# Optimization experiments

Measured on AMD Instinct MI355X. Metric: run time of the kernel, lower is better.

The kernel has to match this reference:

```python
import jax, jax.numpy as jnp
import numpy as np

N = 50000      # nodes
E = 800000     # edges (avg degree 16)
F_IN = 128     # num_features
H1 = 256       # hidden_dims[0]
H2 = 128       # hidden_dims[1]
D_EMB = 64     # embedding_dim
C_CLS = 2      # num_classes
EPS = 1e-5     # BatchNorm eps


def setup_inputs() -> dict:
    key = jax.random.key(0)
    ks = jax.random.split(key, 24)
    f32 = jnp.float32
    def w(k, shape, scale=0.05):
        return jax.random.normal(k, shape, f32) * scale
    inp = {
        "x": jax.random.normal(ks[0], (N, F_IN), f32),
        "edge_index": jax.random.randint(ks[1], (2, E), 0, N, jnp.int32),
        # input_proj
        "Wp": w(ks[2], (F_IN, H1)), "bp": jnp.zeros((H1,), f32),
        # conv1 (SAGEConv): lin_l (neighbors, with bias), lin_r (root, no bias)
        "W1l": w(ks[3], (F_IN, H1)), "b1l": jnp.zeros((H1,), f32), "W1r": w(ks[4], (F_IN, H1)),
        # bn1 (eval mode, running stats)
        "bn1_g": jnp.ones((H1,), f32), "bn1_b": jnp.zeros((H1,), f32),
        "bn1_m": w(ks[5], (H1,), 0.01), "bn1_v": jnp.ones((H1,), f32) + 0.1 * jax.random.uniform(ks[6], (H1,), f32),
        # skip_proj
        "Wsk": w(ks[7], (H1, H2)), "bsk": jnp.zeros((H2,), f32),
        # conv2
        "W2l": w(ks[8], (H1, H2)), "b2l": jnp.zeros((H2,), f32), "W2r": w(ks[9], (H1, H2)),
        # bn2
        "bn2_g": jnp.ones((H2,), f32), "bn2_b": jnp.zeros((H2,), f32),
        "bn2_m": w(ks[10], (H2,), 0.01), "bn2_v": jnp.ones((H2,), f32) + 0.1 * jax.random.uniform(ks[11], (H2,), f32),
        # conv3
        "W3l": w(ks[12], (H2, D_EMB)), "b3l": jnp.zeros((D_EMB,), f32), "W3r": w(ks[13], (H2, D_EMB)),
        # classifier
        "Wc": w(ks[14], (D_EMB, C_CLS)), "bc": jnp.zeros((C_CLS,), f32),
    }
    return inp


def _sage(h, src, dst, Wl, bl, Wr):
    # mean aggregation of source features into destination nodes
    s = jax.ops.segment_sum(h[src], dst, num_segments=N)        # [N, d]
    cnt = jax.ops.segment_sum(jnp.ones((src.shape[0], 1), h.dtype), dst, num_segments=N)
    mean = s / jnp.maximum(cnt, 1.0)
    return mean @ Wl + bl + h @ Wr


def _bn(h, g, b, m, v):
    return (h - m) * jax.lax.rsqrt(v + EPS) * g + b


def reference(x, edge_index, Wp, bp, W1l, b1l, W1r, bn1_g, bn1_b, bn1_m, bn1_v,
              Wsk, bsk, W2l, b2l, W2r, bn2_g, bn2_b, bn2_m, bn2_v,
              W3l, b3l, W3r, Wc, bc):
    src, dst = edge_index[0], edge_index[1]
    identity = x @ Wp + bp                                # input_proj
    h = _sage(x, src, dst, W1l, b1l, W1r)                 # conv1
    h = jax.nn.relu(_bn(h, bn1_g, bn1_b, bn1_m, bn1_v) + identity)
    # dropout is identity in eval mode
    identity = h @ Wsk + bsk                              # skip_proj
    h = _sage(h, src, dst, W2l, b2l, W2r)                 # conv2
    h = jax.nn.relu(_bn(h, bn2_g, bn2_b, bn2_m, bn2_v) + identity)
    emb = _sage(h, src, dst, W3l, b3l, W3r)               # conv3
    logits = emb @ Wc + bc
    return (logits, emb)
```

## Files before the change

kernel.cpp:

```cpp
#include <hip/hip_runtime.h>
#include <hip/hip_fp16.h>

#define NN 50000
#define NE 800000
#define SLN 6250
#define CAP 64
#define BCAP 106496
constexpr float EPSV = 1e-5f;

typedef __attribute__((ext_vector_type(8))) short short8;
typedef __attribute__((ext_vector_type(4))) float f32x4;

__device__ __forceinline__ float bf2f(unsigned short u) {
    return __uint_as_float(((unsigned int)u) << 16);
}
__device__ __forceinline__ unsigned short f2bf(float f) {
    unsigned int x = __float_as_uint(f);
    return (unsigned short)((x + 0x7FFFu + ((x >> 16) & 1u)) >> 16);
}
__device__ __forceinline__ unsigned char f2e5(float f) {
    unsigned short h = __half_as_ushort(__float2half(f));
    unsigned short r = h + 0x7F + ((h >> 8) & 1);
    return (unsigned char)(r >> 8);
}
__device__ __forceinline__ void acc16(float* a, uint4 u) {
#pragma unroll
    for (int q = 0; q < 4; q++) {
        unsigned int x = (q == 0) ? u.x : (q == 1) ? u.y : (q == 2) ? u.z : u.w;
        unsigned int h01 = ((x << 8) & 0xFF00u) | ((x << 16) & 0xFF000000u);
        unsigned int h23 = ((x >> 8) & 0xFF00u) | (x & 0xFF000000u);
        __half2 p01 = *(__half2*)&h01, p23 = *(__half2*)&h23;
        float2 f01 = __half22float2(p01), f23 = __half22float2(p23);
        a[q * 4 + 0] += f01.x; a[q * 4 + 1] += f01.y;
        a[q * 4 + 2] += f23.x; a[q * 4 + 3] += f23.y;
    }
}

__global__ __launch_bounds__(256) void k_bin(const int* __restrict__ src,
                                             const int* __restrict__ dst,
                                             int* __restrict__ binCnt,
                                             int2* __restrict__ binBuf) {
    __shared__ int hcnt[8];
    __shared__ int hbase[8];
    int tid = threadIdx.x;
    if (tid < 8) hcnt[tid] = 0;
    __syncthreads();
    int q = blockIdx.x * 256 + tid;
    bool val = q < NE / 4;
    int4 d = make_int4(0, 0, 0, 0), s = make_int4(0, 0, 0, 0);
    int b0 = 0, b1 = 0, b2 = 0, b3 = 0, r0 = 0, r1 = 0, r2 = 0, r3 = 0;
    if (val) {
        d = ((const int4*)dst)[q];
        s = ((const int4*)src)[q];
        b0 = d.x / SLN; r0 = atomicAdd(&hcnt[b0], 1);
        b1 = d.y / SLN; r1 = atomicAdd(&hcnt[b1], 1);
        b2 = d.z / SLN; r2 = atomicAdd(&hcnt[b2], 1);
        b3 = d.w / SLN; r3 = atomicAdd(&hcnt[b3], 1);
    }
    __syncthreads();
    if (tid < 8) hbase[tid] = atomicAdd(&binCnt[tid], hcnt[tid]);
    __syncthreads();
    if (val) {
        binBuf[(size_t)b0 * BCAP + hbase[b0] + r0] = make_int2(d.x, s.x);
        binBuf[(size_t)b1 * BCAP + hbase[b1] + r1] = make_int2(d.y, s.y);
        binBuf[(size_t)b2 * BCAP + hbase[b2] + r2] = make_int2(d.z, s.z);
        binBuf[(size_t)b3 * BCAP + hbase[b3] + r3] = make_int2(d.w, s.w);
    }
}

__global__ __launch_bounds__(256) void k_scatter2(const int2* __restrict__ binBuf,
                                                  const int* __restrict__ binCnt,
                                                  int* __restrict__ cnt,
                                                  int* __restrict__ csr) {
    int bin = blockIdx.x & 7;
    int lb = blockIdx.x >> 3;
    int n = binCnt[bin];
    const int2* buf = binBuf + (size_t)bin * BCAP;
    for (int i = lb * 256 + threadIdx.x; i < n; i += 128 * 256) {
        int2 p = buf[i];
        int slot = atomicAdd(&cnt[p.x], 1);
        csr[p.x * CAP + slot] = p.y;
    }
}

__device__ void prep1_body(int t, const float* Wp, const float* bp, const float* W1l,
                           const float* b1l, const float* W1r, const float* g, const float* b,
                           const float* m, const float* v, unsigned short* Wf, float* c) {
    int lane = t & 63, f = (t >> 6) & 3, kt = (t >> 8) & 7;
    int nb = t >> 11;
    int col = nb * 64 + f * 16 + (lane & 15);
    int k0 = kt * 32 + (lane >> 4) * 8;
    float A = g[col] * rsqrtf(v[col] + EPSV);
    unsigned short* o = Wf + (size_t)t * 8;
    for (int j = 0; j < 8; j++) {
        int k = k0 + j;
        float w;
        if (k < 128) w = W1l[k * 256 + col] * A;
        else         w = W1r[(k - 128) * 256 + col] * A + Wp[(k - 128) * 256 + col];
        o[j] = f2bf(w);
    }
    if (t < 256) {
        float At = g[t] * rsqrtf(v[t] + EPSV);
        c[t] = b1l[t] * At + (b[t] - m[t] * At) + bp[t];
    }
}

__device__ void prep2_body(int t, const float* Wsk, const float* bsk, const float* W2l,
                           const float* b2l, const float* W2r, const float* g, const float* b,
                           const float* m, const float* v, unsigned short* Wf, float* c) {
    int lane = t & 63, f = (t >> 6) & 3, kt = (t >> 8) & 7, nb = t >> 11;
    int col = nb * 64 + f * 16 + (lane & 15);
    int k0 = kt * 32 + (lane >> 4) * 8;
    unsigned short* o = Wf + (size_t)t * 8;
    if (col < 128) {
        float A = g[col] * rsqrtf(v[col] + EPSV);
        for (int j = 0; j < 8; j++) o[j] = f2bf(W2l[(k0 + j) * 128 + col] * A);
    } else {
        int cc = col - 128;
        float A = g[cc] * rsqrtf(v[cc] + EPSV);
        for (int j = 0; j < 8; j++)
            o[j] = f2bf(W2r[(k0 + j) * 128 + cc] * A + Wsk[(k0 + j) * 128 + cc]);
    }
    if (t < 128) {
        float At = g[t] * rsqrtf(v[t] + EPSV);
        c[t] = b2l[t] * At + (b[t] - m[t] * At) + bsk[t];
    }
}

__device__ void prep3_body(int t, const float* W3l, const float* b3l, const float* W3r,
                           unsigned short* Wf, float* c) {
    int lane = t & 63, f = (t >> 6) & 3, kt = (t >> 8) & 3, nb = t >> 10;
    int col = nb * 64 + f * 16 + (lane & 15);
    int k0 = kt * 32 + (lane >> 4) * 8;
    unsigned short* o = Wf + (size_t)t * 8;
    if (col < 64) {
        for (int j = 0; j < 8; j++) o[j] = f2bf(W3l[(k0 + j) * 64 + col]);
    } else {
        int cc = col - 64;
        for (int j = 0; j < 8; j++) o[j] = f2bf(W3r[(k0 + j) * 64 + cc]);
    }
    if (t < 64) c[t] = b3l[t];
}

__global__ void k_prep_fused(const float* x, unsigned short* xcat, unsigned char* xf8,
                             int* cnt, int* binCnt,
                             const float* Wp, const float* bp,
                             const float* W1l, const float* b1l, const float* W1r,
                             const float* g1, const float* b1, const float* m1, const float* v1,
                             const float* Wsk, const float* bsk,
                             const float* W2l, const float* b2l, const float* W2r,
                             const float* g2, const float* b2, const float* m2, const float* v2,
                             const float* W3l, const float* b3l, const float* W3r,
                             unsigned short* Wf1, unsigned short* Wf2, unsigned short* Wf3,
                             float* c1, float* c2, float* c3) {
    int bb = blockIdx.x;
    if (bb < 6250) {
        int i = bb * 256 + threadIdx.x;
        if (i < NN / 4) ((int4*)cnt)[i] = make_int4(0, 0, 0, 0);
        if (i < 2) ((int4*)binCnt)[i] = make_int4(0, 0, 0, 0);
        if (i >= NN * 128 / 4) return;
        int r = i >> 5, c4 = (i & 31) * 4;
        float4 v = ((const float4*)x)[i];
        ushort4 u = make_ushort4(f2bf(v.x), f2bf(v.y), f2bf(v.z), f2bf(v.w));
        *(ushort4*)&xcat[(size_t)r * 256 + 128 + c4] = u;
        uchar4 u8 = make_uchar4(f2e5(v.x), f2e5(v.y), f2e5(v.z), f2e5(v.w));
        *(uchar4*)&xf8[(size_t)r * 128 + c4] = u8;
    } else if (bb < 6282) {
        prep1_body((bb - 6250) * 256 + threadIdx.x, Wp, bp, W1l, b1l, W1r, g1, b1, m1, v1, Wf1, c1);
    } else if (bb < 6314) {
        prep2_body((bb - 6282) * 256 + threadIdx.x, Wsk, bsk, W2l, b2l, W2r, g2, b2, m2, v2, Wf2, c2);
    } else {
        prep3_body((bb - 6314) * 256 + threadIdx.x, W3l, b3l, W3r, Wf3, c3);
    }
}

template <int K, int TOTN, int MODE>
__global__ __launch_bounds__(256) void k_gemm(const unsigned short* __restrict__ A,
                                              const unsigned short* __restrict__ Wf,
                                              const float* __restrict__ bias,
                                              unsigned short* __restrict__ Out,
                                              unsigned char* __restrict__ Pf8) {
    constexpr int KT = K / 32;
    constexpr int NB = TOTN / 64;
    __shared__ unsigned short Bs[K * 64];
    int tid = threadIdx.x;
    int lane = tid & 63, w = tid >> 6;
    int bm = blockIdx.x;

    int r0 = bm * 128 + w * 32;
    int ra0 = r0 + (lane & 15);
    int ra1 = ra0 + 16;
    if (ra0 >= NN) ra0 = NN - 1;
    if (ra1 >= NN) ra1 = NN - 1;
    const unsigned short* ap0 = A + (size_t)ra0 * K + ((lane >> 4) * 8);
    const unsigned short* ap1 = A + (size_t)ra1 * K + ((lane >> 4) * 8);
    short8 afr0[KT], afr1[KT];
#pragma unroll
    for (int kt = 0; kt < KT; kt++) {
        afr0[kt] = *(const short8*)(ap0 + kt * 32);
        afr1[kt] = *(const short8*)(ap1 + kt * 32);
    }

    int rb = r0 + (lane >> 4) * 4;

    for (int nb = 0; nb < NB; nb++) {
        __syncthreads();
        {
            const float4* srcp = (const float4*)(Wf + (size_t)nb * K * 64);
            float4* dsts = (float4*)Bs;
            for (int i = tid; i < K * 8; i += 256) dsts[i] = srcp[i];
        }
        __syncthreads();

        f32x4 acc[2][4];
#pragma unroll
        for (int i = 0; i < 2; i++)
#pragma unroll
            for (int f = 0; f < 4; f++) acc[i][f] = (f32x4){0.f, 0.f, 0.f, 0.f};
#pragma unroll
        for (int kt = 0; kt < KT; kt++) {
#pragma unroll
            for (int f = 0; f < 4; f++) {
                short8 bfr = *(const short8*)&Bs[((kt * 4 + f) * 64 + lane) * 8];
                acc[0][f] = __builtin_amdgcn_mfma_f32_16x16x32_bf16(afr0[kt], bfr, acc[0][f], 0, 0, 0);
                acc[1][f] = __builtin_amdgcn_mfma_f32_16x16x32_bf16(afr1[kt], bfr, acc[1][f], 0, 0, 0);
            }
        }

        int cc = nb * 64 + (lane & 15);
#pragma unroll
        for (int af = 0; af < 2; af++) {
#pragma unroll
            for (int f = 0; f < 4; f++) {
                float bv = (MODE == 1) ? bias[cc + f * 16] : 0.f;
#pragma unroll
                for (int r = 0; r < 4; r++) {
                    int gr = rb + af * 16 + r;
                    if (gr < NN) {
                        float val = acc[af][f][r];
                        if (MODE == 1) val = fmaxf(val + bv, 0.f);
                        int col = cc + f * 16;
                        if (MODE == 2) {
                            if (col < 128) Pf8[(size_t)gr * 128 + col] = f2e5(val);
                            else           Out[(size_t)gr * 128 + (col - 128)] = f2bf(val);
                        } else {
                            Out[(size_t)gr * TOTN + col] = f2bf(val);
                        }
                    }
                }
            }
        }
    }
}


__global__ __launch_bounds__(256) void k_aggx(const int* __restrict__ cnt,
                                              const int* __restrict__ csr,
                                              const unsigned char* __restrict__ xf8,
                                              unsigned short* __restrict__ xcat) {
    int lane = threadIdx.x & 63, wv = threadIdx.x >> 6;
    int node = blockIdx.x * 4 + wv;
    int deg = cnt[node];
    const int* cp = csr + node * CAP;
    int g = lane >> 3, l8 = lane & 7;
    float a[16];
#pragma unroll
    for (int j = 0; j < 16; j++) a[j] = 0.f;
    const unsigned char* base = xf8 + l8 * 16;
    int e = 0;
    for (; e + 16 <= deg; e += 16) {
        int s0 = cp[e + g], s1 = cp[e + 8 + g];
        uint4 u0 = *(const uint4*)(base + (size_t)s0 * 128);
        uint4 u1 = *(const uint4*)(base + (size_t)s1 * 128);
        acc16(a, u0); acc16(a, u1);
    }
    if (e + g < deg) {
        uint4 u = *(const uint4*)(base + (size_t)cp[e + g] * 128);
        acc16(a, u);
    }
    if (e + 8 + g < deg) {
        uint4 u = *(const uint4*)(base + (size_t)cp[e + 8 + g] * 128);
        acc16(a, u);
    }
#pragma unroll
    for (int j = 0; j < 16; j++) {
        a[j] += __shfl_xor(a[j], 8);
        a[j] += __shfl_xor(a[j], 16);
        a[j] += __shfl_xor(a[j], 32);
    }
    if (lane < 8) {
        float inv = 1.f / (float)max(deg, 1);
        unsigned short o[16];
#pragma unroll
        for (int j = 0; j < 16; j++) o[j] = f2bf(a[j] * inv);
        *(short8*)&xcat[(size_t)node * 256 + lane * 16] = *(short8*)&o[0];
        *(short8*)&xcat[(size_t)node * 256 + lane * 16 + 8] = *(short8*)&o[8];
    }
}

__global__ __launch_bounds__(256) void k_agg2(const unsigned char* __restrict__ pf8,
                                              const unsigned short* __restrict__ r2,
                                              const int* __restrict__ cnt,
                                              const int* __restrict__ csr,
                                              const float* __restrict__ c,
                                              unsigned short* __restrict__ h2) {
    int lane = threadIdx.x & 63, wv = threadIdx.x >> 6;
    int node = blockIdx.x * 4 + wv;
    int deg = cnt[node];
    const int* cp = csr + node * CAP;
    int g = lane >> 3, l8 = lane & 7;
    float a[16];
#pragma unroll
    for (int j = 0; j < 16; j++) a[j] = 0.f;
    const unsigned char* base = pf8 + l8 * 16;
    int e = 0;
    for (; e + 16 <= deg; e += 16) {
        int s0 = cp[e + g], s1 = cp[e + 8 + g];
        uint4 u0 = *(const uint4*)(base + (size_t)s0 * 128);
        uint4 u1 = *(const uint4*)(base + (size_t)s1 * 128);
        acc16(a, u0); acc16(a, u1);
    }
    if (e + g < deg) {
        uint4 u = *(const uint4*)(base + (size_t)cp[e + g] * 128);
        acc16(a, u);
    }
    if (e + 8 + g < deg) {
        uint4 u = *(const uint4*)(base + (size_t)cp[e + 8 + g] * 128);
        acc16(a, u);
    }
#pragma unroll
    for (int j = 0; j < 16; j++) {
        a[j] += __shfl_xor(a[j], 8);
        a[j] += __shfl_xor(a[j], 16);
        a[j] += __shfl_xor(a[j], 32);
    }
    if (lane < 8) {
        float inv = 1.f / (float)max(deg, 1);
        short8 rA = *(const short8*)&r2[(size_t)node * 128 + lane * 16];
        short8 rB = *(const short8*)&r2[(size_t)node * 128 + lane * 16 + 8];
        const float* cpb = c + lane * 16;
        unsigned short o[16];
#pragma unroll
        for (int j = 0; j < 8; j++)
            o[j] = f2bf(fmaxf(a[j] * inv + bf2f(rA[j]) + cpb[j], 0.f));
#pragma unroll
        for (int j = 0; j < 8; j++)
            o[8 + j] = f2bf(fmaxf(a[8 + j] * inv + bf2f(rB[j]) + cpb[8 + j], 0.f));
        *(short8*)&h2[(size_t)node * 128 + lane * 16] = *(short8*)&o[0];
        *(short8*)&h2[(size_t)node * 128 + lane * 16 + 8] = *(short8*)&o[8];
    }
}

__global__ __launch_bounds__(256) void k_agg_final(const unsigned short* __restrict__ G,
                                                   const int* __restrict__ cnt,
                                                   const int* __restrict__ csr,
                                                   const float* __restrict__ c,
                                                   const float* __restrict__ Wc,
                                                   const float* __restrict__ bc,
                                                   float* __restrict__ outbuf) {
    int lane = threadIdx.x & 63, wv = threadIdx.x >> 6;
    int node = blockIdx.x * 4 + wv;
    int deg = cnt[node];
    const int* cp = csr + node * CAP;
    int g = lane >> 3, l8 = lane & 7;
    float a[8];
#pragma unroll
    for (int j = 0; j < 8; j++) a[j] = 0.f;
    const unsigned short* base = G + l8 * 8;
    int e = 0;
    for (; e + 32 <= deg; e += 32) {
        int s0 = cp[e + g], s1 = cp[e + 8 + g], s2 = cp[e + 16 + g], s3 = cp[e + 24 + g];
        short8 u0 = *(const short8*)(base + (size_t)s0 * 128);
        short8 u1 = *(const short8*)(base + (size_t)s1 * 128);
        short8 u2 = *(const short8*)(base + (size_t)s2 * 128);
        short8 u3 = *(const short8*)(base + (size_t)s3 * 128);
#pragma unroll
        for (int j = 0; j < 8; j++)
            a[j] += (bf2f(u0[j]) + bf2f(u1[j])) + (bf2f(u2[j]) + bf2f(u3[j]));
    }
    for (; e + 8 <= deg; e += 8) {
        short8 u = *(const short8*)(base + (size_t)cp[e + g] * 128);
#pragma unroll
        for (int j = 0; j < 8; j++) a[j] += bf2f(u[j]);
    }
    if (e + g < deg) {
        short8 u = *(const short8*)(base + (size_t)cp[e + g] * 128);
#pragma unroll
        for (int j = 0; j < 8; j++) a[j] += bf2f(u[j]);
    }
#pragma unroll
    for (int j = 0; j < 8; j++) {
        a[j] += __shfl_xor(a[j], 8);
        a[j] += __shfl_xor(a[j], 16);
        a[j] += __shfl_xor(a[j], 32);
    }
    float l0 = 0.f, l1 = 0.f;
    if (lane < 8) {
        float inv = 1.f / (float)max(deg, 1);
        short8 r = *(const short8*)&G[(size_t)node * 128 + 64 + l8 * 8];
        const float* cpb = c + l8 * 8;
        float v[8];
#pragma unroll
        for (int j = 0; j < 8; j++) v[j] = a[j] * inv + bf2f(r[j]) + cpb[j];
        float* emb = outbuf + 2 * (size_t)NN;
        *(float4*)&emb[(size_t)node * 64 + l8 * 8] = make_float4(v[0], v[1], v[2], v[3]);
        *(float4*)&emb[(size_t)node * 64 + l8 * 8 + 4] = make_float4(v[4], v[5], v[6], v[7]);
        int c0 = l8 * 8;
#pragma unroll
        for (int j = 0; j < 8; j++) {
            l0 += v[j] * Wc[2 * (c0 + j)];
            l1 += v[j] * Wc[2 * (c0 + j) + 1];
        }
    }
    l0 += __shfl_xor(l0, 1); l1 += __shfl_xor(l1, 1);
    l0 += __shfl_xor(l0, 2); l1 += __shfl_xor(l1, 2);
    l0 += __shfl_xor(l0, 4); l1 += __shfl_xor(l1, 4);
    if (lane == 0) {
        outbuf[(size_t)node * 2 + 0] = l0 + bc[0];
        outbuf[(size_t)node * 2 + 1] = l1 + bc[1];
    }
}

extern "C" void kernel_launch(void* const* d_in, const int* in_sizes, int n_in,
                              void* d_out, int out_size, void* d_ws, size_t ws_size,
                              hipStream_t stream) {
    const float* x    = (const float*)d_in[0];
    const int*   ei   = (const int*)d_in[1];
    const float* Wp   = (const float*)d_in[2];
    const float* bp   = (const float*)d_in[3];
    const float* W1l  = (const float*)d_in[4];
    const float* b1l  = (const float*)d_in[5];
    const float* W1r  = (const float*)d_in[6];
    const float* bn1g = (const float*)d_in[7];
    const float* bn1b = (const float*)d_in[8];
    const float* bn1m = (const float*)d_in[9];
    const float* bn1v = (const float*)d_in[10];
    const float* Wsk  = (const float*)d_in[11];
    const float* bsk  = (const float*)d_in[12];
    const float* W2l  = (const float*)d_in[13];
    const float* b2l  = (const float*)d_in[14];
    const float* W2r  = (const float*)d_in[15];
    const float* bn2g = (const float*)d_in[16];
    const float* bn2b = (const float*)d_in[17];
    const float* bn2m = (const float*)d_in[18];
    const float* bn2v = (const float*)d_in[19];
    const float* W3l  = (const float*)d_in[20];
    const float* b3l  = (const float*)d_in[21];
    const float* W3r  = (const float*)d_in[22];
    const float* Wc   = (const float*)d_in[23];
    const float* bc   = (const float*)d_in[24];

    const int* src = ei;
    const int* dst = ei + NE;

    char* ws = (char*)d_ws;
    size_t o = 0;
    auto alloc = [&](size_t b) -> char* {
        char* p = ws + o;
        o = (o + b + 255) & ~(size_t)255;
        return p;
    };
    int* cnt    = (int*)alloc((size_t)NN * 4);
    int* binCnt = (int*)alloc(64);
    int* csr    = (int*)alloc((size_t)NN * CAP * 4);
    unsigned char*  xf8  = (unsigned char*)alloc((size_t)NN * 128);
    unsigned short* xcat = (unsigned short*)alloc((size_t)NN * 256 * 2);
    unsigned short* h1   = (unsigned short*)alloc((size_t)NN * 256 * 2);
    unsigned char*  pf8  = (unsigned char*)alloc((size_t)NN * 128);
    unsigned short* r2   = (unsigned short*)alloc((size_t)NN * 128 * 2);
    unsigned short* h2   = (unsigned short*)alloc((size_t)NN * 128 * 2);
    unsigned short* G3   = (unsigned short*)alloc((size_t)NN * 128 * 2);
    unsigned short* Wf1  = (unsigned short*)alloc((size_t)256 * 256 * 2);
    unsigned short* Wf2  = (unsigned short*)alloc((size_t)256 * 256 * 2);
    unsigned short* Wf3  = (unsigned short*)alloc((size_t)128 * 128 * 2);
    float* c1 = (float*)alloc(256 * 4);
    float* c2 = (float*)alloc(128 * 4);
    float* c3 = (float*)alloc(64 * 4);
    int2* binBuf = (int2*)G3;

    float* outbuf = (float*)d_out;

    k_prep_fused<<<6322, 256, 0, stream>>>(x, xcat, xf8, cnt, binCnt,
                                           Wp, bp, W1l, b1l, W1r, bn1g, bn1b, bn1m, bn1v,
                                           Wsk, bsk, W2l, b2l, W2r, bn2g, bn2b, bn2m, bn2v,
                                           W3l, b3l, W3r, Wf1, Wf2, Wf3, c1, c2, c3);

    k_bin<<<782, 256, 0, stream>>>(src, dst, binCnt, binBuf);
    k_scatter2<<<1024, 256, 0, stream>>>(binBuf, binCnt, cnt, csr);

    k_aggx<<<12500, 256, 0, stream>>>(cnt, csr, xf8, xcat);
    k_gemm<256, 256, 1><<<391, 256, 0, stream>>>(xcat, Wf1, c1, h1, nullptr);

    k_gemm<256, 256, 2><<<391, 256, 0, stream>>>(h1, Wf2, nullptr, r2, pf8);
    k_agg2<<<12500, 256, 0, stream>>>(pf8, r2, cnt, csr, c2, h2);

    k_gemm<128, 128, 0><<<391, 256, 0, stream>>>(h2, Wf3, nullptr, G3, nullptr);
    k_agg_final<<<12500, 256, 0, stream>>>(G3, cnt, csr, c3, Wc, bc, outbuf);
}
```

Before: 210.8 us.

## Fuse conv1 and conv2 GEMMs into one kernel keeping h1 in LDS

Adds a kernel that runs the layer-1 GEMM (bias+ReLU) for a 64-row tile, stores the bf16 h1 tile in padded shared memory, and feeds it straight into the layer-2 GEMM that writes pf8/r2. This removes the global round trip of the N×256 bf16 h1 buffer and one kernel launch. In exchange the tiles are smaller (64 rows per block, 782 blocks), both weight matrices are re-streamed through LDS per block, LDS use per block rises, and the generic GEMM loses its MODE-specific epilogues.

New measurement: 200.2 us (median of 2 runs). 1.05x faster.

```diff
diff --git a/kernel.cpp b/kernel.cpp
--- a/kernel.cpp
+++ b/kernel.cpp
@@ -174,6 +174,106 @@
     }
 }
 
+__global__ __launch_bounds__(256) void k_gemm12(const unsigned short* __restrict__ xcat,
+                                                const unsigned short* __restrict__ Wf1,
+                                                const float* __restrict__ c1,
+                                                const unsigned short* __restrict__ Wf2,
+                                                unsigned short* __restrict__ r2,
+                                                unsigned char* __restrict__ pf8) {
+    constexpr int KT = 8;
+    constexpr int HS = 272;
+    __shared__ unsigned short Bs[256 * 64];
+    __shared__ unsigned short hs[64 * HS];
+    int tid = threadIdx.x;
+    int lane = tid & 63, w = tid >> 6;
+    int bm = blockIdx.x;
+    int rbase = bm * 64 + w * 16;
+
+    int ra = rbase + (lane & 15);
+    if (ra >= NN) ra = NN - 1;
+    const unsigned short* ap = xcat + (size_t)ra * 256 + ((lane >> 4) * 8);
+    short8 afr[KT];
+#pragma unroll
+    for (int kt = 0; kt < KT; kt++) afr[kt] = *(const short8*)(ap + kt * 32);
+
+    int hrow0 = w * 16 + (lane >> 4) * 4;
+
+    for (int nb = 0; nb < 4; nb++) {
+        __syncthreads();
+        {
+            const float4* srcp = (const float4*)(Wf1 + (size_t)nb * 256 * 64);
+            float4* dsts = (float4*)Bs;
+            for (int i = tid; i < 256 * 8; i += 256) dsts[i] = srcp[i];
+        }
+        __syncthreads();
+        f32x4 acc[4];
+#pragma unroll
+        for (int f = 0; f < 4; f++) acc[f] = (f32x4){0.f, 0.f, 0.f, 0.f};
+#pragma unroll
+        for (int kt = 0; kt < KT; kt++) {
+#pragma unroll
+            for (int f = 0; f < 4; f++) {
+                short8 bfr = *(const short8*)&Bs[((kt * 4 + f) * 64 + lane) * 8];
+                acc[f] = __builtin_amdgcn_mfma_f32_16x16x32_bf16(afr[kt], bfr, acc[f], 0, 0, 0);
+            }
+        }
+        int cc = nb * 64 + (lane & 15);
+#pragma unroll
+        for (int f = 0; f < 4; f++) {
+            int col = cc + f * 16;
+            float bv = c1[col];
+#pragma unroll
+            for (int r = 0; r < 4; r++) {
+                float val = fmaxf(acc[f][r] + bv, 0.f);
+                hs[(hrow0 + r) * HS + col] = f2bf(val);
+            }
+        }
+    }
+
+    short8 a2[KT];
+    {
+        const unsigned short* hp = &hs[(w * 16 + (lane & 15)) * HS + ((lane >> 4) * 8)];
+#pragma unroll
+        for (int kt = 0; kt < KT; kt++) a2[kt] = *(const short8*)(hp + kt * 32);
+    }
+
+    int gr0 = rbase + (lane >> 4) * 4;
+    for (int nb = 0; nb < 4; nb++) {
+        __syncthreads();
+        {
+            const float4* srcp = (const float4*)(Wf2 + (size_t)nb * 256 * 64);
+            float4* dsts = (float4*)Bs;
+            for (int i = tid; i < 256 * 8; i += 256) dsts[i] = srcp[i];
+        }
+        __syncthreads();
+        f32x4 acc[4];
+#pragma unroll
+        for (int f = 0; f < 4; f++) acc[f] = (f32x4){0.f, 0.f, 0.f, 0.f};
+#pragma unroll
+        for (int kt = 0; kt < KT; kt++) {
+#pragma unroll
+            for (int f = 0; f < 4; f++) {
+                short8 bfr = *(const short8*)&Bs[((kt * 4 + f) * 64 + lane) * 8];
+                acc[f] = __builtin_amdgcn_mfma_f32_16x16x32_bf16(a2[kt], bfr, acc[f], 0, 0, 0);
+            }
+        }
+        int cc = nb * 64 + (lane & 15);
+#pragma unroll
+        for (int f = 0; f < 4; f++) {
+            int col = cc + f * 16;
+#pragma unroll
+            for (int r = 0; r < 4; r++) {
+                int gr = gr0 + r;
+                if (gr < NN) {
+                    float val = acc[f][r];
+                    if (col < 128) pf8[(size_t)gr * 128 + col] = f2e5(val);
+                    else           r2[(size_t)gr * 128 + (col - 128)] = f2bf(val);
+                }
+            }
+        }
+    }
+}
+
 template <int K, int TOTN, int MODE>
 __global__ __launch_bounds__(256) void k_gemm(const unsigned short* __restrict__ A,
                                               const unsigned short* __restrict__ Wf,
@@ -232,20 +332,12 @@
         for (int af = 0; af < 2; af++) {
 #pragma unroll
             for (int f = 0; f < 4; f++) {
-                float bv = (MODE == 1) ? bias[cc + f * 16] : 0.f;
 #pragma unroll
                 for (int r = 0; r < 4; r++) {
                     int gr = rb + af * 16 + r;
                     if (gr < NN) {
                         float val = acc[af][f][r];
-                        if (MODE == 1) val = fmaxf(val + bv, 0.f);
-                        int col = cc + f * 16;
-                        if (MODE == 2) {
-                            if (col < 128) Pf8[(size_t)gr * 128 + col] = f2e5(val);
-                            else           Out[(size_t)gr * 128 + (col - 128)] = f2bf(val);
-                        } else {
-                            Out[(size_t)gr * TOTN + col] = f2bf(val);
-                        }
+                        Out[(size_t)gr * TOTN + cc + f * 16] = f2bf(val);
                     }
                 }
             }
@@ -465,7 +557,6 @@
     int* csr    = (int*)alloc((size_t)NN * CAP * 4);
     unsigned char*  xf8  = (unsigned char*)alloc((size_t)NN * 128);
     unsigned short* xcat = (unsigned short*)alloc((size_t)NN * 256 * 2);
-    unsigned short* h1   = (unsigned short*)alloc((size_t)NN * 256 * 2);
     unsigned char*  pf8  = (unsigned char*)alloc((size_t)NN * 128);
     unsigned short* r2   = (unsigned short*)alloc((size_t)NN * 128 * 2);
     unsigned short* h2   = (unsigned short*)alloc((size_t)NN * 128 * 2);
@@ -489,9 +580,8 @@
     k_scatter2<<<1024, 256, 0, stream>>>(binBuf, binCnt, cnt, csr);
 
     k_aggx<<<12500, 256, 0, stream>>>(cnt, csr, xf8, xcat);
-    k_gemm<256, 256, 1><<<391, 256, 0, stream>>>(xcat, Wf1, c1, h1, nullptr);
-
-    k_gemm<256, 256, 2><<<391, 256, 0, stream>>>(h1, Wf2, nullptr, r2, pf8);
+
+    k_gemm12<<<782, 256, 0, stream>>>(xcat, Wf1, c1, Wf2, r2, pf8);
     k_agg2<<<12500, 256, 0, stream>>>(pf8, r2, cnt, csr, c2, h2);
 
     k_gemm<128, 128, 0><<<391, 256, 0, stream>>>(h2, Wf3, nullptr, G3, nullptr);
```

## Fuse edge binning into prep kernel and split GEMM column blocks across grid

Applied to the files above, without the earlier changes.

Folds the edge-binning kernel into the fused prep kernel as extra blocks, zeroing binCnt with a memset beforehand. The two 256-wide GEMMs now put each 64-column block in its own grid.y slice instead of looping over it, which gives four times as many blocks at the cost of reloading A fragments per slice. The third GEMM becomes a dedicated kernel with 64-row tiles to double its block count. The aim is more parallelism and one fewer launch, in exchange for redundant A reads and an extra memset.

Result: slower. 222.6 us (+5.6%).

```diff
diff --git a/kernel.cpp b/kernel.cpp
--- a/kernel.cpp
+++ b/kernel.cpp
@@ -33,38 +33,6 @@
         float2 f01 = __half22float2(p01), f23 = __half22float2(p23);
         a[q * 4 + 0] += f01.x; a[q * 4 + 1] += f01.y;
         a[q * 4 + 2] += f23.x; a[q * 4 + 3] += f23.y;
-    }
-}
-
-__global__ __launch_bounds__(256) void k_bin(const int* __restrict__ src,
-                                             const int* __restrict__ dst,
-                                             int* __restrict__ binCnt,
-                                             int2* __restrict__ binBuf) {
-    __shared__ int hcnt[8];
-    __shared__ int hbase[8];
-    int tid = threadIdx.x;
-    if (tid < 8) hcnt[tid] = 0;
-    __syncthreads();
-    int q = blockIdx.x * 256 + tid;
-    bool val = q < NE / 4;
-    int4 d = make_int4(0, 0, 0, 0), s = make_int4(0, 0, 0, 0);
-    int b0 = 0, b1 = 0, b2 = 0, b3 = 0, r0 = 0, r1 = 0, r2 = 0, r3 = 0;
-    if (val) {
-        d = ((const int4*)dst)[q];
-        s = ((const int4*)src)[q];
-        b0 = d.x / SLN; r0 = atomicAdd(&hcnt[b0], 1);
-        b1 = d.y / SLN; r1 = atomicAdd(&hcnt[b1], 1);
-        b2 = d.z / SLN; r2 = atomicAdd(&hcnt[b2], 1);
-        b3 = d.w / SLN; r3 = atomicAdd(&hcnt[b3], 1);
-    }
-    __syncthreads();
-    if (tid < 8) hbase[tid] = atomicAdd(&binCnt[tid], hcnt[tid]);
-    __syncthreads();
-    if (val) {
-        binBuf[(size_t)b0 * BCAP + hbase[b0] + r0] = make_int2(d.x, s.x);
-        binBuf[(size_t)b1 * BCAP + hbase[b1] + r1] = make_int2(d.y, s.y);
-        binBuf[(size_t)b2 * BCAP + hbase[b2] + r2] = make_int2(d.z, s.z);
-        binBuf[(size_t)b3 * BCAP + hbase[b3] + r3] = make_int2(d.w, s.w);
     }
 }
 
@@ -144,6 +112,7 @@
 
 __global__ void k_prep_fused(const float* x, unsigned short* xcat, unsigned char* xf8,
                              int* cnt, int* binCnt,
+                             const int* src, const int* dst, int2* binBuf,
                              const float* Wp, const float* bp,
                              const float* W1l, const float* b1l, const float* W1r,
                              const float* g1, const float* b1, const float* m1, const float* v1,
@@ -153,11 +122,13 @@
                              const float* W3l, const float* b3l, const float* W3r,
                              unsigned short* Wf1, unsigned short* Wf2, unsigned short* Wf3,
                              float* c1, float* c2, float* c3) {
+    __shared__ int hcnt[8];
+    __shared__ int hbase[8];
     int bb = blockIdx.x;
+    int tid = threadIdx.x;
     if (bb < 6250) {
-        int i = bb * 256 + threadIdx.x;
+        int i = bb * 256 + tid;
         if (i < NN / 4) ((int4*)cnt)[i] = make_int4(0, 0, 0, 0);
-        if (i < 2) ((int4*)binCnt)[i] = make_int4(0, 0, 0, 0);
         if (i >= NN * 128 / 4) return;
         int r = i >> 5, c4 = (i & 31) * 4;
         float4 v = ((const float4*)x)[i];
@@ -166,11 +137,35 @@
         uchar4 u8 = make_uchar4(f2e5(v.x), f2e5(v.y), f2e5(v.z), f2e5(v.w));
         *(uchar4*)&xf8[(size_t)r * 128 + c4] = u8;
     } else if (bb < 6282) {
-        prep1_body((bb - 6250) * 256 + threadIdx.x, Wp, bp, W1l, b1l, W1r, g1, b1, m1, v1, Wf1, c1);
+        prep1_body((bb - 6250) * 256 + tid, Wp, bp, W1l, b1l, W1r, g1, b1, m1, v1, Wf1, c1);
     } else if (bb < 6314) {
-        prep2_body((bb - 6282) * 256 + threadIdx.x, Wsk, bsk, W2l, b2l, W2r, g2, b2, m2, v2, Wf2, c2);
+        prep2_body((bb - 6282) * 256 + tid, Wsk, bsk, W2l, b2l, W2r, g2, b2, m2, v2, Wf2, c2);
+    } else if (bb < 6322) {
+        prep3_body((bb - 6314) * 256 + tid, W3l, b3l, W3r, Wf3, c3);
     } else {
-        prep3_body((bb - 6314) * 256 + threadIdx.x, W3l, b3l, W3r, Wf3, c3);
+        if (tid < 8) hcnt[tid] = 0;
+        __syncthreads();
+        int q = (bb - 6322) * 256 + tid;
+        bool val = q < NE / 4;
+        int4 d = make_int4(0, 0, 0, 0), s = make_int4(0, 0, 0, 0);
+        int b0 = 0, b1i = 0, b2i = 0, b3i = 0, r0 = 0, r1 = 0, r2 = 0, r3 = 0;
+        if (val) {
+            d = ((const int4*)dst)[q];
+            s = ((const int4*)src)[q];
+            b0 = d.x / SLN; r0 = atomicAdd(&hcnt[b0], 1);
+            b1i = d.y / SLN; r1 = atomicAdd(&hcnt[b1i], 1);
+            b2i = d.z / SLN; r2 = atomicAdd(&hcnt[b2i], 1);
+            b3i = d.w / SLN; r3 = atomicAdd(&hcnt[b3i], 1);
+        }
+        __syncthreads();
+        if (tid < 8) hbase[tid] = atomicAdd(&binCnt[tid], hcnt[tid]);
+        __syncthreads();
+        if (val) {
+            binBuf[(size_t)b0 * BCAP + hbase[b0] + r0] = make_int2(d.x, s.x);
+            binBuf[(size_t)b1i * BCAP + hbase[b1i] + r1] = make_int2(d.y, s.y);
+            binBuf[(size_t)b2i * BCAP + hbase[b2i] + r2] = make_int2(d.z, s.z);
+            binBuf[(size_t)b3i * BCAP + hbase[b3i] + r3] = make_int2(d.w, s.w);
+        }
     }
 }
 
@@ -181,11 +176,10 @@
                                               unsigned short* __restrict__ Out,
                                               unsigned char* __restrict__ Pf8) {
     constexpr int KT = K / 32;
-    constexpr int NB = TOTN / 64;
     __shared__ unsigned short Bs[K * 64];
     int tid = threadIdx.x;
     int lane = tid & 63, w = tid >> 6;
-    int bm = blockIdx.x;
+    int bm = blockIdx.x, nb = blockIdx.y;
 
     int r0 = bm * 128 + w * 32;
     int ra0 = r0 + (lane & 15);
@@ -201,53 +195,98 @@
         afr1[kt] = *(const short8*)(ap1 + kt * 32);
     }
 
+    {
+        const float4* srcp = (const float4*)(Wf + (size_t)nb * K * 64);
+        float4* dsts = (float4*)Bs;
+        for (int i = tid; i < K * 8; i += 256) dsts[i] = srcp[i];
+    }
+    __syncthreads();
+
+    f32x4 acc[2][4];
+#pragma unroll
+    for (int i = 0; i < 2; i++)
+#pragma unroll
+        for (int f = 0; f < 4; f++) acc[i][f] = (f32x4){0.f, 0.f, 0.f, 0.f};
+#pragma unroll
+    for (int kt = 0; kt < KT; kt++) {
+#pragma unroll
+        for (int f = 0; f < 4; f++) {
+            short8 bfr = *(const short8*)&Bs[((kt * 4 + f) * 64 + lane) * 8];
+            acc[0][f] = __builtin_amdgcn_mfma_f32_16x16x32_bf16(afr0[kt], bfr, acc[0][f], 0, 0, 0);
+            acc[1][f] = __builtin_amdgcn_mfma_f32_16x16x32_bf16(afr1[kt], bfr, acc[1][f], 0, 0, 0);
+        }
+    }
+
+    int cc = nb * 64 + (lane & 15);
     int rb = r0 + (lane >> 4) * 4;
-
-    for (int nb = 0; nb < NB; nb++) {
+#pragma unroll
+    for (int af = 0; af < 2; af++) {
+#pragma unroll
+        for (int f = 0; f < 4; f++) {
+            int col = cc + f * 16;
+            float bv = (MODE == 1) ? bias[col] : 0.f;
+#pragma unroll
+            for (int r = 0; r < 4; r++) {
+                int gr = rb + af * 16 + r;
+                if (gr < NN) {
+                    float val = acc[af][f][r];
+                    if (MODE == 1) {
+                        val = fmaxf(val + bv, 0.f);
+                        Out[(size_t)gr * TOTN + col] = f2bf(val);
+                    } else {
+                        if (col < 128) Pf8[(size_t)gr * 128 + col] = f2e5(val);
+                        else           Out[(size_t)gr * 128 + (col - 128)] = f2bf(val);
+                    }
+                }
+            }
+        }
+    }
+}
+
+__global__ __launch_bounds__(256) void k_gemm3(const unsigned short* __restrict__ h2,
+                                               const unsigned short* __restrict__ Wf3,
+                                               unsigned short* __restrict__ G3) {
+    constexpr int KT = 4;
+    __shared__ unsigned short Bs[128 * 64];
+    int tid = threadIdx.x;
+    int lane = tid & 63, w = tid >> 6;
+    int bm = blockIdx.x;
+
+    int ra = bm * 64 + w * 16 + (lane & 15);
+    if (ra >= NN) ra = NN - 1;
+    const unsigned short* ap = h2 + (size_t)ra * 128 + ((lane >> 4) * 8);
+    short8 afr[KT];
+#pragma unroll
+    for (int kt = 0; kt < KT; kt++) afr[kt] = *(const short8*)(ap + kt * 32);
+
+    int gr0 = bm * 64 + w * 16 + (lane >> 4) * 4;
+
+    for (int nb = 0; nb < 2; nb++) {
         __syncthreads();
         {
-            const float4* srcp = (const float4*)(Wf + (size_t)nb * K * 64);
+            const float4* srcp = (const float4*)(Wf3 + (size_t)nb * 128 * 64);
             float4* dsts = (float4*)Bs;
-            for (int i = tid; i < K * 8; i += 256) dsts[i] = srcp[i];
+            for (int i = tid; i < 128 * 8; i += 256) dsts[i] = srcp[i];
         }
         __syncthreads();
-
-        f32x4 acc[2][4];
-#pragma unroll
-        for (int i = 0; i < 2; i++)
-#pragma unroll
-            for (int f = 0; f < 4; f++) acc[i][f] = (f32x4){0.f, 0.f, 0.f, 0.f};
+        f32x4 acc[4];
+#pragma unroll
+        for (int f = 0; f < 4; f++) acc[f] = (f32x4){0.f, 0.f, 0.f, 0.f};
 #pragma unroll
         for (int kt = 0; kt < KT; kt++) {
 #pragma unroll
             for (int f = 0; f < 4; f++) {
                 short8 bfr = *(const short8*)&Bs[((kt * 4 + f) * 64 + lane) * 8];
-                acc[0][f] = __builtin_amdgcn_mfma_f32_16x16x32_bf16(afr0[kt], bfr, acc[0][f], 0, 0, 0);
-                acc[1][f] = __builtin_amdgcn_mfma_f32_16x16x32_bf16(afr1[kt], bfr, acc[1][f], 0, 0, 0);
+                acc[f] = __builtin_amdgcn_mfma_f32_16x16x32_bf16(afr[kt], bfr, acc[f], 0, 0, 0);
             }
         }
-
         int cc = nb * 64 + (lane & 15);
 #pragma unroll
-        for (int af = 0; af < 2; af++) {
-#pragma unroll
-            for (int f = 0; f < 4; f++) {
-                float bv = (MODE == 1) ? bias[cc + f * 16] : 0.f;
-#pragma unroll
-                for (int r = 0; r < 4; r++) {
-                    int gr = rb + af * 16 + r;
-                    if (gr < NN) {
-                        float val = acc[af][f][r];
-                        if (MODE == 1) val = fmaxf(val + bv, 0.f);
-                        int col = cc + f * 16;
-                        if (MODE == 2) {
-                            if (col < 128) Pf8[(size_t)gr * 128 + col] = f2e5(val);
-                            else           Out[(size_t)gr * 128 + (col - 128)] = f2bf(val);
-                        } else {
-                            Out[(size_t)gr * TOTN + col] = f2bf(val);
-                        }
-                    }
-                }
+        for (int f = 0; f < 4; f++) {
+#pragma unroll
+            for (int r = 0; r < 4; r++) {
+                int gr = gr0 + r;
+                if (gr < NN) G3[(size_t)gr * 128 + cc + f * 16] = f2bf(acc[f][r]);
             }
         }
     }
@@ -480,20 +519,20 @@
 
     float* outbuf = (float*)d_out;
 
-    k_prep_fused<<<6322, 256, 0, stream>>>(x, xcat, xf8, cnt, binCnt,
+    hipMemsetAsync(binCnt, 0, 64, stream);
+    k_prep_fused<<<7104, 256, 0, stream>>>(x, xcat, xf8, cnt, binCnt, src, dst, binBuf,
                                            Wp, bp, W1l, b1l, W1r, bn1g, bn1b, bn1m, bn1v,
                                            Wsk, bsk, W2l, b2l, W2r, bn2g, bn2b, bn2m, bn2v,
                                            W3l, b3l, W3r, Wf1, Wf2, Wf3, c1, c2, c3);
 
-    k_bin<<<782, 256, 0, stream>>>(src, dst, binCnt, binBuf);
     k_scatter2<<<1024, 256, 0, stream>>>(binBuf, binCnt, cnt, csr);
 
     k_aggx<<<12500, 256, 0, stream>>>(cnt, csr, xf8, xcat);
-    k_gemm<256, 256, 1><<<391, 256, 0, stream>>>(xcat, Wf1, c1, h1, nullptr);
-
-    k_gemm<256, 256, 2><<<391, 256, 0, stream>>>(h1, Wf2, nullptr, r2, pf8);
+    k_gemm<256, 256, 1><<<dim3(391, 4), 256, 0, stream>>>(xcat, Wf1, c1, h1, nullptr);
+
+    k_gemm<256, 256, 2><<<dim3(391, 4), 256, 0, stream>>>(h1, Wf2, nullptr, r2, pf8);
     k_agg2<<<12500, 256, 0, stream>>>(pf8, r2, cnt, csr, c2, h2);
 
-    k_gemm<128, 128, 0><<<391, 256, 0, stream>>>(h2, Wf3, nullptr, G3, nullptr);
+    k_gemm3<<<782, 256, 0, stream>>>(h2, Wf3, G3);
     k_agg_final<<<12500, 256, 0, stream>>>(G3, cnt, csr, c3, Wc, bc, outbuf);
 }
```
